# Kernel tuning notes

Measured on AMD Instinct MI355X. Metric: run time of the kernel, lower is better.

## Reference

```python
import jax, jax.numpy as jnp
import numpy as np

GRID_SIZE = 5
SPLINE_ORDER = 3
COUPLING = 0.05
LN_EPS = 1e-5
BATCH = 1024
IN_DIM = 2048
HIDDEN = [4096, 4096, 2048]


def _knots():
    k = SPLINE_ORDER
    return np.concatenate([np.full(k, -1.0), np.linspace(-1.0, 1.0, GRID_SIZE + 1), np.full(k, 1.0)])


def bspline_basis(t):
    # Replicates the module's partial in-place Cox-de Boor recursion exactly:
    # after the loops, cols[0..4] are degree-3, col 5 degree-2, col 6 degree-1, col 7 degree-0.
    knots = _knots()
    k = SPLINE_ORDER
    n = len(knots) - k - 1  # 8
    cols = [jnp.where((t >= knots[i]) & (t < knots[i + 1]), 1.0, 0.0).astype(t.dtype)
            for i in range(min(n, len(knots) - 1))]
    for degree in range(1, min(k + 1, n)):
        for i in range(n - degree):
            denom1 = knots[i + degree] - knots[i]
            denom2 = knots[i + degree + 1] - knots[i + 1]
            term1 = ((t - knots[i]) / denom1) * cols[i] if denom1 > 1e-10 else 0.0
            term2 = (((knots[i + degree + 1] - t) / denom2) * cols[i + 1]
                     if (denom2 > 1e-10 and i + 1 < n) else 0.0)
            cols[i] = term1 + term2
    return jnp.stack(cols, axis=-1)  # [..., n]


def kan_activation(x, control_points, reg_weights):
    # x: [B, D]; control_points: [D, grid+order+1]; reg_weights: [D]
    t = jnp.tanh(x)
    basis = bspline_basis(t)  # [B, D, n]
    m = min(basis.shape[-1], control_points.shape[1])  # min(8, 9) = 8
    spline = jnp.einsum('bdn,dn->bd', basis[..., :m], control_points[:, :m])
    return jnp.clip(spline * reg_weights[None, :], -10.0, 10.0)


def _generators():
    sx = np.array([[0., 1.], [1., 0.]], np.float32)
    sy = np.array([[0., -1.], [1., 0.]], np.float32)
    sz = np.array([[1., 0.], [0., -1.]], np.float32)
    return np.stack([sx, sy, sz, np.eye(2, dtype=np.float32)])  # [4,2,2]

GENS = jnp.asarray(_generators())
GEN_DIAG = jnp.asarray(np.stack([np.diagonal(g) for g in _generators()]))  # [4,2]


def noncommutative_transform(x):
    # pairs of the flattened tensor, generator index cycles mod 4
    shape = x.shape
    flat = x.reshape(-1)
    P = flat.shape[0] // 2
    vec = flat[:2 * P].reshape(P, 2)
    ng = GENS.shape[0]
    if P % ng == 0:
        v = vec.reshape(P // ng, ng, 2)                      # [Q, 4, 2]
        gv = jnp.einsum('gij,qgj->qgi', GENS, v)
        vg = v * GEN_DIAG[None, :, :]
        comm = jnp.clip(gv - vg, -1.0, 1.0)
        out = (v + COUPLING * comm).reshape(-1)
    else:
        G = GENS[jnp.arange(P) % ng]
        gv = jnp.einsum('pij,pj->pi', G, vec)
        vg = vec * jnp.diagonal(G, axis1=-2, axis2=-1)
        comm = jnp.clip(gv - vg, -1.0, 1.0)
        out = (vec + COUPLING * comm).reshape(-1)
    if flat.shape[0] % 2 == 1:
        out = jnp.concatenate([out, flat[-1:]])
    return out.reshape(shape)


def setup_inputs() -> dict:
    key = jax.random.key(0)
    ks = jax.random.split(key, 16)
    inp = {'x': jax.random.normal(ks[0], (BATCH, IN_DIM), jnp.float32)}
    prev = IN_DIM
    ncp = GRID_SIZE + SPLINE_ORDER + 1  # 9
    for li, h in enumerate(HIDDEN, start=1):
        kw, kb, kc = jax.random.split(ks[li], 3)
        inp[f'W{li}'] = jax.random.normal(kw, (h, prev), jnp.float32) / np.sqrt(prev)
        inp[f'b{li}'] = jnp.zeros((h,), jnp.float32)
        inp[f'cp{li}'] = jax.random.normal(kc, (h, ncp), jnp.float32) * 0.1
        inp[f'rw{li}'] = jnp.full((h,), 0.5, jnp.float32)
        prev = h
    inp['W_out'] = jax.random.normal(ks[10], (IN_DIM, prev), jnp.float32) / np.sqrt(prev)
    inp['b_out'] = jnp.zeros((IN_DIM,), jnp.float32)
    return inp


def reference(x, W1, b1, cp1, rw1, W2, b2, cp2, rw2, W3, b3, cp3, rw3, W_out, b_out):
    # F.layer_norm over feature dim, no affine
    mu = jnp.mean(x, axis=-1, keepdims=True)
    var = jnp.var(x, axis=-1, keepdims=True)
    cur = (x - mu) / jnp.sqrt(var + LN_EPS)
    for W, b, cp, rw in ((W1, b1, cp1, rw1), (W2, b2, cp2, rw2), (W3, b3, cp3, rw3)):
        lin = cur @ W.T + b
        kan = kan_activation(lin, cp, rw)
        cur = noncommutative_transform(kan)  # dropout = identity in eval
    return cur @ W_out.T + b_out
```

## Files before the change

### kernel.cpp

```cpp
#include <hip/hip_runtime.h>

typedef __attribute__((ext_vector_type(8))) short bf16x8;
typedef __attribute__((ext_vector_type(4))) float f32x4;

__device__ __forceinline__ float b2f(unsigned short u) {
    union { unsigned int i; float f; } x; x.i = ((unsigned int)u) << 16; return x.f;
}
__device__ __forceinline__ unsigned short f2b(float f) {
    union { float f; unsigned int i; } x; x.f = f;
    unsigned int r = x.i + 0x7fffu + ((x.i >> 16) & 1u);
    return (unsigned short)(r >> 16);
}

__device__ __forceinline__ void gl16(unsigned short* l, const unsigned short* g) {
    __builtin_amdgcn_global_load_lds((__attribute__((address_space(1))) void*)g,
                                     (__attribute__((address_space(3))) void*)l, 16, 0, 0);
}

__device__ __forceinline__ float kan_spline(float t, const float* cpf, float rwf) {
    float c3 = (t >= -1.0f && t < -0.6f) ? 1.0f : 0.0f;
    float c4 = (t >= -0.6f && t < -0.2f) ? 1.0f : 0.0f;
    float c5 = (t >= -0.2f && t <  0.2f) ? 1.0f : 0.0f;
    float c6 = (t >=  0.2f && t <  0.6f) ? 1.0f : 0.0f;
    float c7 = (t >=  0.6f && t <  1.0f) ? 1.0f : 0.0f;
    float d2 = (-0.6f - t) * 2.5f * c3;
    float d3 = (t + 1.0f) * 2.5f * c3 + (-0.2f - t) * 2.5f * c4;
    float d4 = (t + 0.6f) * 2.5f * c4 + ( 0.2f - t) * 2.5f * c5;
    float d5 = (t + 0.2f) * 2.5f * c5 + ( 0.6f - t) * 2.5f * c6;
    float d6 = (t - 0.2f) * 2.5f * c6 + ( 1.0f - t) * 2.5f * c7;
    float e1 = (-0.6f - t) * 2.5f  * d2;
    float e2 = (t + 1.0f) * 2.5f  * d2 + (-0.2f - t) * 1.25f * d3;
    float e3 = (t + 1.0f) * 1.25f * d3 + ( 0.2f - t) * 1.25f * d4;
    float e4 = (t + 0.6f) * 1.25f * d4 + ( 0.6f - t) * 1.25f * d5;
    float e5 = (t + 0.2f) * 1.25f * d5 + ( 1.0f - t) * 1.25f * d6;
    const float r12 = 1.0f / 1.2f;
    float f0 = (-0.6f - t) * 2.5f  * e1;
    float f1 = (t + 1.0f) * 2.5f  * e1 + (-0.2f - t) * 1.25f * e2;
    float f2 = (t + 1.0f) * 1.25f * e2 + ( 0.2f - t) * r12   * e3;
    float f3 = (t + 1.0f) * r12   * e3 + ( 0.6f - t) * r12   * e4;
    float f4 = (t + 0.6f) * r12   * e4 + ( 1.0f - t) * r12   * e5;
    float sp = f0*cpf[0] + f1*cpf[1] + f2*cpf[2] + f3*cpf[3] + f4*cpf[4]
             + e5*cpf[5] + d6*cpf[6] + c7*cpf[7];
    float v = sp * rwf;
    return fminf(fmaxf(v, -10.0f), 10.0f);
}

__global__ void ln_stats_kernel(const float* __restrict__ x,
                                float* __restrict__ mu, float* __restrict__ rstd) {
    const int row = blockIdx.x;
    const float* p = x + (size_t)row * 2048 + threadIdx.x * 8;
    double s = 0.0, q = 0.0;
#pragma unroll
    for (int i = 0; i < 8; ++i) { float v = p[i]; s += v; q += (double)v * v; }
    for (int o = 32; o > 0; o >>= 1) { s += __shfl_down(s, o, 64); q += __shfl_down(q, o, 64); }
    __shared__ double shs[4], shq[4];
    const int lane = threadIdx.x & 63, w = threadIdx.x >> 6;
    if (lane == 0) { shs[w] = s; shq[w] = q; }
    __syncthreads();
    if (threadIdx.x == 0) {
        double S = shs[0] + shs[1] + shs[2] + shs[3];
        double Q = shq[0] + shq[1] + shq[2] + shq[3];
        double m = S / 2048.0;
        double var = Q / 2048.0 - m * m;
        mu[row] = (float)m;
        rstd[row] = (float)(1.0 / sqrt(var + 1e-5));
    }
}

__global__ void rowsum_kernel(const float* __restrict__ W,
                              float* __restrict__ S, int K) {
    const int lane = threadIdx.x & 63, w = threadIdx.x >> 6;
    const int row = blockIdx.x * 4 + w;
    const float* p = W + (size_t)row * K;
    double s = 0.0;
    for (int c = lane * 8; c < K; c += 512) {
#pragma unroll
        for (int i = 0; i < 8; ++i) s += p[c + i];
    }
    for (int o = 32; o > 0; o >>= 1) s += __shfl_down(s, o, 64);
    if (lane == 0) S[row] = (float)s;
}

__global__ void split2_kernel(const float* __restrict__ src,
                              unsigned short* __restrict__ dst, int C) {
    const int r = blockIdx.x;
    const int c = threadIdx.x * 8;
    const float* p = src + (size_t)r * C + c;
    float4 u0 = ((const float4*)p)[0];
    float4 u1 = ((const float4*)p)[1];
    float v[8] = {u0.x, u0.y, u0.z, u0.w, u1.x, u1.y, u1.z, u1.w};
    unsigned short hi[8], lo[8];
#pragma unroll
    for (int i = 0; i < 8; ++i) {
        hi[i] = f2b(v[i]);
        lo[i] = f2b(v[i] - b2f(hi[i]));
    }
    unsigned short* d = dst + (size_t)r * 2 * C + c;
    *(uint4*)d = *(const uint4*)hi;
    *(uint4*)(d + C) = *(const uint4*)lo;
}

__global__ void cvt_kernel(const float* __restrict__ src,
                           unsigned short* __restrict__ dst) {
    const size_t i = ((size_t)blockIdx.x * 256 + threadIdx.x) * 8;
    float4 u0 = ((const float4*)(src + i))[0];
    float4 u1 = ((const float4*)(src + i))[1];
    float v[8] = {u0.x, u0.y, u0.z, u0.w, u1.x, u1.y, u1.z, u1.w};
    unsigned short t[8];
#pragma unroll
    for (int q = 0; q < 8; ++q) t[q] = f2b(v[q]);
    *(uint4*)(dst + i) = *(const uint4*)t;
}

template <int EPI>
__global__ __launch_bounds__(256, 2)
void gemm_kan2(const unsigned short* __restrict__ Ab,
               const unsigned short* __restrict__ Bb,
               const float* __restrict__ bias, const float* __restrict__ cp,
               const float* __restrict__ rw, const float* __restrict__ mu,
               const float* __restrict__ rstd, const float* __restrict__ S1,
               void* __restrict__ outp,
               int Nld, int n0, int Ktot, int lda, int ldb)
{
    constexpr int BM = 64, BN = 128, BK = 64;
    constexpr int ASZ = BM * BK;
    constexpr int BUF = ASZ + BN * BK;
    __shared__ unsigned short lds[3 * BUF];

    const int tid  = threadIdx.x;
    const int lane = tid & 63;
    const int wid  = tid >> 6;

    const int gx = gridDim.x;
    int flat = blockIdx.y * gx + blockIdx.x;
    const int nwg = gx * gridDim.y;
    if ((nwg & 7) == 0) flat = (flat & 7) * (nwg >> 3) + (flat >> 3);
    const int bm = (flat % gx) * BM;
    const int bn = (flat / gx) * BN;

    const int wmo = (wid >> 1) * 32;
    const int wno = (wid & 1) * 64;
    const int fr = lane & 15;
    const int kq = lane >> 4;
    const int sxr = fr & 7;

    const int uA0 = (wid << 7) + lane;
    const int uA1 = uA0 + 64;
    const int uB0 = (wid << 8) + lane;
    const int uB1 = uB0 + 64, uB2 = uB0 + 128, uB3 = uB0 + 192;
#define SRCOL(u) (((((u) & 7) ^ (((u) >> 3) & 7))) << 3)
    const size_t aoff0 = (size_t)(bm + (uA0 >> 3)) * lda + SRCOL(uA0);
    const size_t aoff1 = (size_t)(bm + (uA1 >> 3)) * lda + SRCOL(uA1);
    const size_t boff0 = (size_t)(bn + (uB0 >> 3)) * ldb + SRCOL(uB0);
    const size_t boff1 = (size_t)(bn + (uB1 >> 3)) * ldb + SRCOL(uB1);
    const size_t boff2 = (size_t)(bn + (uB2 >> 3)) * ldb + SRCOL(uB2);
    const size_t boff3 = (size_t)(bn + (uB3 >> 3)) * ldb + SRCOL(uB3);
#undef SRCOL

    f32x4 acc[2][4] = {};

#define STAGE(BSEL, AK, BKK) do {                                     \
    unsigned short* lA_ = &lds[(BSEL) * BUF];                         \
    unsigned short* lB_ = lA_ + ASZ;                                  \
    gl16(lA_ + uA0 * 8, Ab + aoff0 + (AK));                           \
    gl16(lA_ + uA1 * 8, Ab + aoff1 + (AK));                           \
    gl16(lB_ + uB0 * 8, Bb + boff0 + (BKK));                          \
    gl16(lB_ + uB1 * 8, Bb + boff1 + (BKK));                          \
    gl16(lB_ + uB2 * 8, Bb + boff2 + (BKK));                          \
    gl16(lB_ + uB3 * 8, Bb + boff3 + (BKK));                          \
} while (0)

    const int nt = Ktot / BK;
    STAGE(0, 0, 0);
    STAGE(1, BK, BK);

    for (int t = 0; t < nt; ++t) {
        if (t + 1 < nt) asm volatile("s_waitcnt vmcnt(6)" ::: "memory");
        else            asm volatile("s_waitcnt vmcnt(0)" ::: "memory");
        __builtin_amdgcn_s_barrier();
        __builtin_amdgcn_sched_barrier(0);
        if (t + 2 < nt) {
            const int kn = (t + 2) * BK;
            int ak = kn, bk = kn;
            if (EPI == 0) {
                ak = (kn < 4096) ? kn : kn - 4096;
                bk = (kn < 2048) ? kn : kn - 2048;
            }
            STAGE((t + 2) % 3, ak, bk);
        }
        const unsigned short* cl = &lds[(t % 3) * BUF];
#pragma unroll
        for (int s = 0; s < 2; ++s) {
            const int sl = ((((s << 2) + kq) ^ sxr)) << 3;
            bf16x8 aF[2], bF[4];
#pragma unroll
            for (int i = 0; i < 2; ++i)
                aF[i] = *(const bf16x8*)&cl[(wmo + i * 16 + fr) * BK + sl];
#pragma unroll
            for (int j = 0; j < 4; ++j)
                bF[j] = *(const bf16x8*)&cl[ASZ + (wno + j * 16 + fr) * BK + sl];
#pragma unroll
            for (int i = 0; i < 2; ++i)
#pragma unroll
                for (int j = 0; j < 4; ++j)
                    acc[i][j] = __builtin_amdgcn_mfma_f32_16x16x32_bf16(aF[i], bF[j], acc[i][j], 0, 0, 0);
        }
    }
#undef STAGE

    const int rowg = (lane >> 4) * 4;
#pragma unroll
    for (int j = 0; j < 4; ++j) {
        const int n = n0 + bn + wno + j * 16 + fr;
        const float bs = bias[n];
        float cpf[8], rwf = 0.0f, s1 = 0.0f;
        if (EPI < 2) {
#pragma unroll
            for (int q = 0; q < 8; ++q) cpf[q] = cp[(size_t)n * 9 + q];
            rwf = rw[n];
        }
        if (EPI == 0) s1 = S1[n];
        const int s = n & 7;
#pragma unroll
        for (int i = 0; i < 2; ++i) {
            const int m0 = bm + wmo + i * 16 + rowg;
#pragma unroll
            for (int r = 0; r < 4; ++r) {
                const int m = m0 + r;
                float v = acc[i][j][r];
                if (EPI == 0) v = (v - mu[m] * s1) * rstd[m] + bs;
                else          v += bs;
                if (EPI < 2) {
                    v = kan_spline(tanhf(v), cpf, rwf);
                    float p = __shfl_xor(v, 1, 64);
                    p = fminf(fmaxf(p, -1.0f), 1.0f);
                    if (s < 4) v += ((s == 2) ? -0.05f : 0.05f) * p;
                }
                if (EPI == 2) ((float*)outp)[(size_t)m * Nld + n] = v;
                else ((unsigned short*)outp)[(size_t)m * Nld + n] = f2b(v);
            }
        }
    }
}

template <int EPI, int BSRC>
__global__ __launch_bounds__(256, 2)
void gemm_kan(const void* __restrict__ Av, const void* __restrict__ Bv,
              const float* __restrict__ bias, const float* __restrict__ cp,
              const float* __restrict__ rw, const float* __restrict__ mu,
              const float* __restrict__ rstd, const float* __restrict__ S1,
              void* __restrict__ outp,
              int Nld, int n0, int Ktot, int lda, int ldb)
{
    constexpr int BM = 64, BN = 64, BK = 64, LDP = 72;
    constexpr bool SPL = (BSRC == 2);
    constexpr int OFF_B  = BM * LDP;
    constexpr int OFF_LO = (BM + BN) * LDP;
    __shared__ unsigned short lds[(SPL ? 2 : 1) * (BM + BN) * LDP];

    const int tid  = threadIdx.x;
    const int lane = tid & 63;
    const int wid  = tid >> 6;
    const int bm = blockIdx.x * BM;
    const int bn = blockIdx.y * BN;
    const int wmo = (wid >> 1) * 32;
    const int wno = (wid & 1) * 32;
    const int fr = lane & 15;
    const int kq = lane >> 4;
    const int sar = tid >> 3, sac = (tid & 7) << 3;
    const int sfr = tid >> 2, sfc = (tid & 3) << 4;

    f32x4 acc[2][2] = {};

    uint4 pA0 = {}, pA1 = {}, pB0 = {}, pB1 = {};
    const unsigned short* Ab = (const unsigned short*)Av;
    const unsigned short* Bb = (const unsigned short*)Bv;
    const size_t a0 = (size_t)(bm + sar) * lda + sac;
    const size_t a1 = (size_t)(bm + 32 + sar) * lda + sac;
    const size_t b0 = (size_t)(bn + sar) * ldb + sac;
    const size_t b1 = (size_t)(bn + 32 + sar) * ldb + sac;
    if constexpr (BSRC == 0) {
        pA0 = *(const uint4*)(Ab + a0);
        pA1 = *(const uint4*)(Ab + a1);
        pB0 = *(const uint4*)(Bb + b0);
        pB1 = *(const uint4*)(Bb + b1);
    }

    for (int k0 = 0; k0 < Ktot; k0 += BK) {
        if constexpr (BSRC == 0) {
            *(uint4*)&lds[sar * LDP + sac] = pA0;
            *(uint4*)&lds[(32 + sar) * LDP + sac] = pA1;
            *(uint4*)&lds[OFF_B + sar * LDP + sac] = pB0;
            *(uint4*)&lds[OFF_B + (32 + sar) * LDP + sac] = pB1;
        } else {
            {
                const float* g = (const float*)Bv + (size_t)(bn + sfr) * ldb + k0 + sfc;
                float4 u0 = ((const float4*)g)[0];
                float4 u1 = ((const float4*)g)[1];
                float4 u2 = ((const float4*)g)[2];
                float4 u3 = ((const float4*)g)[3];
                float v[16] = {u0.x,u0.y,u0.z,u0.w, u1.x,u1.y,u1.z,u1.w,
                               u2.x,u2.y,u2.z,u2.w, u3.x,u3.y,u3.z,u3.w};
                unsigned short hi[16], lo[16];
#pragma unroll
                for (int i = 0; i < 16; ++i) {
                    hi[i] = f2b(v[i]);
                    if (SPL) lo[i] = f2b(v[i] - b2f(hi[i]));
                }
                unsigned short* d = &lds[OFF_B + sfr * LDP + sfc];
                ((uint4*)d)[0] = *(const uint4*)&hi[0];
                ((uint4*)d)[1] = *(const uint4*)&hi[8];
                if constexpr (SPL) {
                    unsigned short* dl = d + OFF_LO;
                    ((uint4*)dl)[0] = *(const uint4*)&lo[0];
                    ((uint4*)dl)[1] = *(const uint4*)&lo[8];
                }
            }
            if constexpr (SPL) {
                const float* g = (const float*)Av + (size_t)(bm + sfr) * lda + k0 + sfc;
                float4 u0 = ((const float4*)g)[0];
                float4 u1 = ((const float4*)g)[1];
                float4 u2 = ((const float4*)g)[2];
                float4 u3 = ((const float4*)g)[3];
                float v[16] = {u0.x,u0.y,u0.z,u0.w, u1.x,u1.y,u1.z,u1.w,
                               u2.x,u2.y,u2.z,u2.w, u3.x,u3.y,u3.z,u3.w};
                unsigned short hi[16], lo[16];
#pragma unroll
                for (int i = 0; i < 16; ++i) {
                    hi[i] = f2b(v[i]);
                    lo[i] = f2b(v[i] - b2f(hi[i]));
                }
                unsigned short* d = &lds[sfr * LDP + sfc];
                ((uint4*)d)[0] = *(const uint4*)&hi[0];
                ((uint4*)d)[1] = *(const uint4*)&hi[8];
                unsigned short* dl = d + OFF_LO;
                ((uint4*)dl)[0] = *(const uint4*)&lo[0];
                ((uint4*)dl)[1] = *(const uint4*)&lo[8];
            } else {
                *(uint4*)&lds[sar * LDP + sac] = *(const uint4*)(Ab + a0 + k0);
                *(uint4*)&lds[(32 + sar) * LDP + sac] = *(const uint4*)(Ab + a1 + k0);
            }
        }
        __syncthreads();
        if constexpr (BSRC == 0) {
            if (k0 + BK < Ktot) {
                const int kn = k0 + BK;
                const int ak = (EPI == 0) ? (kn < 4096 ? kn : kn - 4096) : kn;
                const int bk = (EPI == 0) ? (kn < 2048 ? kn : kn - 2048) : kn;
                pA0 = *(const uint4*)(Ab + a0 + ak);
                pA1 = *(const uint4*)(Ab + a1 + ak);
                pB0 = *(const uint4*)(Bb + b0 + bk);
                pB1 = *(const uint4*)(Bb + b1 + bk);
            }
        }
#pragma unroll
        for (int s = 0; s < 2; ++s) {
            const int cc = (s * 4 + kq) << 3;
            bf16x8 aF[2], bF[2];
#pragma unroll
            for (int i = 0; i < 2; ++i)
                aF[i] = *(const bf16x8*)&lds[(wmo + i * 16 + fr) * LDP + cc];
#pragma unroll
            for (int j = 0; j < 2; ++j)
                bF[j] = *(const bf16x8*)&lds[OFF_B + (wno + j * 16 + fr) * LDP + cc];
#pragma unroll
            for (int i = 0; i < 2; ++i)
#pragma unroll
                for (int j = 0; j < 2; ++j)
                    acc[i][j] = __builtin_amdgcn_mfma_f32_16x16x32_bf16(aF[i], bF[j], acc[i][j], 0, 0, 0);
            if constexpr (SPL) {
                bf16x8 aL[2], bL[2];
#pragma unroll
                for (int i = 0; i < 2; ++i)
                    aL[i] = *(const bf16x8*)&lds[OFF_LO + (wmo + i * 16 + fr) * LDP + cc];
#pragma unroll
                for (int i = 0; i < 2; ++i)
#pragma unroll
                    for (int j = 0; j < 2; ++j)
                        acc[i][j] = __builtin_amdgcn_mfma_f32_16x16x32_bf16(aL[i], bF[j], acc[i][j], 0, 0, 0);
#pragma unroll
                for (int j = 0; j < 2; ++j)
                    bL[j] = *(const bf16x8*)&lds[OFF_LO + OFF_B + (wno + j * 16 + fr) * LDP + cc];
#pragma unroll
                for (int i = 0; i < 2; ++i)
#pragma unroll
                    for (int j = 0; j < 2; ++j)
                        acc[i][j] = __builtin_amdgcn_mfma_f32_16x16x32_bf16(aF[i], bL[j], acc[i][j], 0, 0, 0);
            }
        }
        __syncthreads();
    }

    const int rowg = (lane >> 4) * 4;
#pragma unroll
    for (int j = 0; j < 2; ++j) {
        const int n = n0 + bn + wno + j * 16 + fr;
        const float bs = bias[n];
        float cpf[8], rwf = 0.0f, s1 = 0.0f;
        if (EPI < 2) {
#pragma unroll
            for (int q = 0; q < 8; ++q) cpf[q] = cp[(size_t)n * 9 + q];
            rwf = rw[n];
        }
        if (EPI == 0) s1 = S1[n];
        const int s = n & 7;
#pragma unroll
        for (int i = 0; i < 2; ++i) {
            const int m0 = bm + wmo + i * 16 + rowg;
#pragma unroll
            for (int r = 0; r < 4; ++r) {
                const int m = m0 + r;
                float v = acc[i][j][r];
                if (EPI == 0) v = (v - mu[m] * s1) * rstd[m] + bs;
                else          v += bs;
                if (EPI < 2) {
                    v = kan_spline(tanhf(v), cpf, rwf);
                    float p = __shfl_xor(v, 1, 64);
                    p = fminf(fmaxf(p, -1.0f), 1.0f);
                    if (s < 4) v += ((s == 2) ? -0.05f : 0.05f) * p;
                }
                if (EPI == 2) ((float*)outp)[(size_t)m * Nld + n] = v;
                else ((unsigned short*)outp)[(size_t)m * Nld + n] = f2b(v);
            }
        }
    }
}

extern "C" void kernel_launch(void* const* d_in, const int* in_sizes, int n_in,
                              void* d_out, int out_size, void* d_ws, size_t ws_size,
                              hipStream_t stream) {
    const float* x    = (const float*)d_in[0];
    const float* W1   = (const float*)d_in[1];
    const float* b1   = (const float*)d_in[2];
    const float* cp1  = (const float*)d_in[3];
    const float* rw1  = (const float*)d_in[4];
    const float* W2   = (const float*)d_in[5];
    const float* b2   = (const float*)d_in[6];
    const float* cp2  = (const float*)d_in[7];
    const float* rw2  = (const float*)d_in[8];
    const float* W3   = (const float*)d_in[9];
    const float* b3   = (const float*)d_in[10];
    const float* cp3  = (const float*)d_in[11];
    const float* rw3  = (const float*)d_in[12];
    const float* Wout = (const float*)d_in[13];
    const float* bout = (const float*)d_in[14];

    char* ws = (char*)d_ws;
    float* mu   = (float*)(ws);
    float* rstd = (float*)(ws + 4096);
    float* S1   = (float*)(ws + 8192);
    unsigned short* A2 = (unsigned short*)(ws + 32768);
    unsigned short* A3 = (unsigned short*)(ws + 32768 + 8388608);
    unsigned short* A4 = A2;
    unsigned short* Asplit = A3;
    unsigned short* Wb = (unsigned short*)(ws + 32768 + 2 * 8388608);
    const size_t NEED_FULL = 32768 + 2 * 8388608 + 33554432;
    const size_t NEED_HALF = 32768 + 2 * 8388608 + 16777216;

    ln_stats_kernel<<<1024, 256, 0, stream>>>(x, mu, rstd);
    rowsum_kernel<<<1024, 256, 0, stream>>>(W1, S1, 2048);

    if (ws_size >= NEED_FULL) {
        split2_kernel<<<1024, 256, 0, stream>>>(x, Asplit, 2048);
        split2_kernel<<<4096, 256, 0, stream>>>(W1, Wb, 2048);
        gemm_kan2<0><<<dim3(16, 32), 256, 0, stream>>>(
            Asplit, Wb, b1, cp1, rw1, mu, rstd, S1, A2, 4096, 0, 6144, 4096, 4096);
        cvt_kernel<<<8192, 256, 0, stream>>>(W2, Wb);
        gemm_kan2<1><<<dim3(16, 32), 256, 0, stream>>>(
            A2, Wb, b2, cp2, rw2, nullptr, nullptr, nullptr, A3, 4096, 0, 4096, 4096, 4096);
        cvt_kernel<<<4096, 256, 0, stream>>>(W3, Wb);
        gemm_kan2<1><<<dim3(16, 16), 256, 0, stream>>>(
            A3, Wb, b3, cp3, rw3, nullptr, nullptr, nullptr, A4, 2048, 0, 4096, 4096, 4096);
        cvt_kernel<<<2048, 256, 0, stream>>>(Wout, Wb);
        gemm_kan2<2><<<dim3(16, 16), 256, 0, stream>>>(
            A4, Wb, bout, nullptr, nullptr, nullptr, nullptr, nullptr, d_out, 2048, 0, 2048, 2048, 2048);
    } else if (ws_size >= NEED_HALF) {
        split2_kernel<<<1024, 256, 0, stream>>>(x, Asplit, 2048);
        for (int h = 0; h < 2; ++h) {
            split2_kernel<<<2048, 256, 0, stream>>>(W1 + (size_t)h * 2048 * 2048, Wb, 2048);
            gemm_kan2<0><<<dim3(16, 16), 256, 0, stream>>>(
                Asplit, Wb, b1, cp1, rw1, mu, rstd, S1, A2, 4096, h * 2048, 6144, 4096, 4096);
        }
        for (int h = 0; h < 2; ++h) {
            cvt_kernel<<<4096, 256, 0, stream>>>(W2 + (size_t)h * 2048 * 4096, Wb);
            gemm_kan2<1><<<dim3(16, 16), 256, 0, stream>>>(
                A2, Wb, b2, cp2, rw2, nullptr, nullptr, nullptr, A3, 4096, h * 2048, 4096, 4096, 4096);
        }
        cvt_kernel<<<4096, 256, 0, stream>>>(W3, Wb);
        gemm_kan2<1><<<dim3(16, 16), 256, 0, stream>>>(
            A3, Wb, b3, cp3, rw3, nullptr, nullptr, nullptr, A4, 2048, 0, 4096, 4096, 4096);
        cvt_kernel<<<2048, 256, 0, stream>>>(Wout, Wb);
        gemm_kan2<2><<<dim3(16, 16), 256, 0, stream>>>(
            A4, Wb, bout, nullptr, nullptr, nullptr, nullptr, nullptr, d_out, 2048, 0, 2048, 2048, 2048);
    } else {
        gemm_kan<0, 2><<<dim3(16, 64), 256, 0, stream>>>(
            x, W1, b1, cp1, rw1, mu, rstd, S1, A2, 4096, 0, 2048, 2048, 2048);
        gemm_kan<1, 1><<<dim3(16, 64), 256, 0, stream>>>(
            A2, W2, b2, cp2, rw2, nullptr, nullptr, nullptr, A3, 4096, 0, 4096, 4096, 4096);
        gemm_kan<1, 1><<<dim3(16, 32), 256, 0, stream>>>(
            A3, W3, b3, cp3, rw3, nullptr, nullptr, nullptr, A4, 2048, 0, 4096, 4096, 4096);
        gemm_kan<2, 1><<<dim3(16, 32), 256, 0, stream>>>(
            A4, Wout, bout, nullptr, nullptr, nullptr, nullptr, nullptr, d_out, 2048, 0, 2048, 2048, 2048);
    }
}
```

Baseline: 395.8 us.

## Enlarge GEMM tile to 128x128 with double-buffered LDS pipeline

The bf16 GEMM+KAN kernel's M tile grows from 64 to 128, so each wave computes a 64x64 sub-tile with 16 MFMA accumulators and the grid halves in x. The LDS pipeline drops from three stages to two to fit the larger tile, and each iteration now waits for all outstanding loads (vmcnt(0)) before computing. The aim is more data reuse per LDS load and fewer workgroups re-reading B. The cost is more registers per thread, fewer workgroups, and less overlap between memory loads and compute.

```diff
diff --git a/kernel.cpp b/kernel.cpp
--- a/kernel.cpp
+++ b/kernel.cpp
@@ -114,7 +114,7 @@
 
 template <int EPI>
 __global__ __launch_bounds__(256, 2)
-void gemm_kan2(const unsigned short* __restrict__ Ab,
+void gemm_kan3(const unsigned short* __restrict__ Ab,
                const unsigned short* __restrict__ Bb,
                const float* __restrict__ bias, const float* __restrict__ cp,
                const float* __restrict__ rw, const float* __restrict__ mu,
@@ -122,10 +122,10 @@
                void* __restrict__ outp,
                int Nld, int n0, int Ktot, int lda, int ldb)
 {
-    constexpr int BM = 64, BN = 128, BK = 64;
+    constexpr int BM = 128, BN = 128, BK = 64;
     constexpr int ASZ = BM * BK;
     constexpr int BUF = ASZ + BN * BK;
-    __shared__ unsigned short lds[3 * BUF];
+    __shared__ unsigned short lds[2 * BUF];
 
     const int tid  = threadIdx.x;
     const int lane = tid & 63;
@@ -138,69 +138,69 @@
     const int bm = (flat % gx) * BM;
     const int bn = (flat / gx) * BN;
 
-    const int wmo = (wid >> 1) * 32;
+    const int wmo = (wid >> 1) * 64;
     const int wno = (wid & 1) * 64;
     const int fr = lane & 15;
     const int kq = lane >> 4;
     const int sxr = fr & 7;
 
-    const int uA0 = (wid << 7) + lane;
-    const int uA1 = uA0 + 64;
-    const int uB0 = (wid << 8) + lane;
-    const int uB1 = uB0 + 64, uB2 = uB0 + 128, uB3 = uB0 + 192;
+    const int u0 = (wid << 8) + lane;
+    const int u1 = u0 + 64, u2 = u0 + 128, u3 = u0 + 192;
 #define SRCOL(u) (((((u) & 7) ^ (((u) >> 3) & 7))) << 3)
-    const size_t aoff0 = (size_t)(bm + (uA0 >> 3)) * lda + SRCOL(uA0);
-    const size_t aoff1 = (size_t)(bm + (uA1 >> 3)) * lda + SRCOL(uA1);
-    const size_t boff0 = (size_t)(bn + (uB0 >> 3)) * ldb + SRCOL(uB0);
-    const size_t boff1 = (size_t)(bn + (uB1 >> 3)) * ldb + SRCOL(uB1);
-    const size_t boff2 = (size_t)(bn + (uB2 >> 3)) * ldb + SRCOL(uB2);
-    const size_t boff3 = (size_t)(bn + (uB3 >> 3)) * ldb + SRCOL(uB3);
+    const size_t aoff0 = (size_t)(bm + (u0 >> 3)) * lda + SRCOL(u0);
+    const size_t aoff1 = (size_t)(bm + (u1 >> 3)) * lda + SRCOL(u1);
+    const size_t aoff2 = (size_t)(bm + (u2 >> 3)) * lda + SRCOL(u2);
+    const size_t aoff3 = (size_t)(bm + (u3 >> 3)) * lda + SRCOL(u3);
+    const size_t boff0 = (size_t)(bn + (u0 >> 3)) * ldb + SRCOL(u0);
+    const size_t boff1 = (size_t)(bn + (u1 >> 3)) * ldb + SRCOL(u1);
+    const size_t boff2 = (size_t)(bn + (u2 >> 3)) * ldb + SRCOL(u2);
+    const size_t boff3 = (size_t)(bn + (u3 >> 3)) * ldb + SRCOL(u3);
 #undef SRCOL
 
-    f32x4 acc[2][4] = {};
+    f32x4 acc[4][4] = {};
 
 #define STAGE(BSEL, AK, BKK) do {                                     \
     unsigned short* lA_ = &lds[(BSEL) * BUF];                         \
     unsigned short* lB_ = lA_ + ASZ;                                  \
-    gl16(lA_ + uA0 * 8, Ab + aoff0 + (AK));                           \
-    gl16(lA_ + uA1 * 8, Ab + aoff1 + (AK));                           \
-    gl16(lB_ + uB0 * 8, Bb + boff0 + (BKK));                          \
-    gl16(lB_ + uB1 * 8, Bb + boff1 + (BKK));                          \
-    gl16(lB_ + uB2 * 8, Bb + boff2 + (BKK));                          \
-    gl16(lB_ + uB3 * 8, Bb + boff3 + (BKK));                          \
+    gl16(lA_ + u0 * 8, Ab + aoff0 + (AK));                            \
+    gl16(lA_ + u1 * 8, Ab + aoff1 + (AK));                            \
+    gl16(lA_ + u2 * 8, Ab + aoff2 + (AK));                            \
+    gl16(lA_ + u3 * 8, Ab + aoff3 + (AK));                            \
+    gl16(lB_ + u0 * 8, Bb + boff0 + (BKK));                           \
+    gl16(lB_ + u1 * 8, Bb + boff1 + (BKK));                           \
+    gl16(lB_ + u2 * 8, Bb + boff2 + (BKK));                           \
+    gl16(lB_ + u3 * 8, Bb + boff3 + (BKK));                           \
 } while (0)
 
     const int nt = Ktot / BK;
     STAGE(0, 0, 0);
-    STAGE(1, BK, BK);
 
     for (int t = 0; t < nt; ++t) {
-        if (t + 1 < nt) asm volatile("s_waitcnt vmcnt(6)" ::: "memory");
-        else            asm volatile("s_waitcnt vmcnt(0)" ::: "memory");
+        asm volatile("s_waitcnt vmcnt(0)" ::: "memory");
         __builtin_amdgcn_s_barrier();
         __builtin_amdgcn_sched_barrier(0);
-        if (t + 2 < nt) {
-            const int kn = (t + 2) * BK;
+        if (t + 1 < nt) {
+            const int kn = (t + 1) * BK;
             int ak = kn, bk = kn;
             if (EPI == 0) {
                 ak = (kn < 4096) ? kn : kn - 4096;
                 bk = (kn < 2048) ? kn : kn - 2048;
             }
-            STAGE((t + 2) % 3, ak, bk);
-        }
-        const unsigned short* cl = &lds[(t % 3) * BUF];
+            STAGE((t + 1) & 1, ak, bk);
+        }
+        const unsigned short* cl = &lds[(t & 1) * BUF];
 #pragma unroll
         for (int s = 0; s < 2; ++s) {
             const int sl = ((((s << 2) + kq) ^ sxr)) << 3;
-            bf16x8 aF[2], bF[4];
-#pragma unroll
-            for (int i = 0; i < 2; ++i)
+            bf16x8 aF[4], bF[4];
+#pragma unroll
+            for (int i = 0; i < 4; ++i)
                 aF[i] = *(const bf16x8*)&cl[(wmo + i * 16 + fr) * BK + sl];
 #pragma unroll
             for (int j = 0; j < 4; ++j)
                 bF[j] = *(const bf16x8*)&cl[ASZ + (wno + j * 16 + fr) * BK + sl];
 #pragma unroll
-            for (int i = 0; i < 2; ++i)
+            for (int i = 0; i < 4; ++i)
 #pragma unroll
                 for (int j = 0; j < 4; ++j)
                     acc[i][j] = __builtin_amdgcn_mfma_f32_16x16x32_bf16(aF[i], bF[j], acc[i][j], 0, 0, 0);
@@ -222,7 +222,7 @@
         if (EPI == 0) s1 = S1[n];
         const int s = n & 7;
 #pragma unroll
-        for (int i = 0; i < 2; ++i) {
+        for (int i = 0; i < 4; ++i) {
             const int m0 = bm + wmo + i * 16 + rowg;
 #pragma unroll
             for (int r = 0; r < 4; ++r) {
@@ -463,34 +463,34 @@
     if (ws_size >= NEED_FULL) {
         split2_kernel<<<1024, 256, 0, stream>>>(x, Asplit, 2048);
         split2_kernel<<<4096, 256, 0, stream>>>(W1, Wb, 2048);
-        gemm_kan2<0><<<dim3(16, 32), 256, 0, stream>>>(
+        gemm_kan3<0><<<dim3(8, 32), 256, 0, stream>>>(
             Asplit, Wb, b1, cp1, rw1, mu, rstd, S1, A2, 4096, 0, 6144, 4096, 4096);
         cvt_kernel<<<8192, 256, 0, stream>>>(W2, Wb);
-        gemm_kan2<1><<<dim3(16, 32), 256, 0, stream>>>(
+        gemm_kan3<1><<<dim3(8, 32), 256, 0, stream>>>(
             A2, Wb, b2, cp2, rw2, nullptr, nullptr, nullptr, A3, 4096, 0, 4096, 4096, 4096);
         cvt_kernel<<<4096, 256, 0, stream>>>(W3, Wb);
-        gemm_kan2<1><<<dim3(16, 16), 256, 0, stream>>>(
+        gemm_kan3<1><<<dim3(8, 16), 256, 0, stream>>>(
             A3, Wb, b3, cp3, rw3, nullptr, nullptr, nullptr, A4, 2048, 0, 4096, 4096, 4096);
         cvt_kernel<<<2048, 256, 0, stream>>>(Wout, Wb);
-        gemm_kan2<2><<<dim3(16, 16), 256, 0, stream>>>(
+        gemm_kan3<2><<<dim3(8, 16), 256, 0, stream>>>(
             A4, Wb, bout, nullptr, nullptr, nullptr, nullptr, nullptr, d_out, 2048, 0, 2048, 2048, 2048);
     } else if (ws_size >= NEED_HALF) {
         split2_kernel<<<1024, 256, 0, stream>>>(x, Asplit, 2048);
         for (int h = 0; h < 2; ++h) {
             split2_kernel<<<2048, 256, 0, stream>>>(W1 + (size_t)h * 2048 * 2048, Wb, 2048);
-            gemm_kan2<0><<<dim3(16, 16), 256, 0, stream>>>(
+            gemm_kan3<0><<<dim3(8, 16), 256, 0, stream>>>(
                 Asplit, Wb, b1, cp1, rw1, mu, rstd, S1, A2, 4096, h * 2048, 6144, 4096, 4096);
         }
         for (int h = 0; h < 2; ++h) {
             cvt_kernel<<<4096, 256, 0, stream>>>(W2 + (size_t)h * 2048 * 4096, Wb);
-            gemm_kan2<1><<<dim3(16, 16), 256, 0, stream>>>(
+            gemm_kan3<1><<<dim3(8, 16), 256, 0, stream>>>(
                 A2, Wb, b2, cp2, rw2, nullptr, nullptr, nullptr, A3, 4096, h * 2048, 4096, 4096, 4096);
         }
         cvt_kernel<<<4096, 256, 0, stream>>>(W3, Wb);
-        gemm_kan2<1><<<dim3(16, 16), 256, 0, stream>>>(
+        gemm_kan3<1><<<dim3(8, 16), 256, 0, stream>>>(
             A3, Wb, b3, cp3, rw3, nullptr, nullptr, nullptr, A4, 2048, 0, 4096, 4096, 4096);
         cvt_kernel<<<2048, 256, 0, stream>>>(Wout, Wb);
-        gemm_kan2<2><<<dim3(16, 16), 256, 0, stream>>>(
+        gemm_kan3<2><<<dim3(8, 16), 256, 0, stream>>>(
             A4, Wb, bout, nullptr, nullptr, nullptr, nullptr, nullptr, d_out, 2048, 0, 2048, 2048, 2048);
     } else {
         gemm_kan<0, 2><<<dim3(16, 64), 256, 0, stream>>>(
```

New measurement: 460.7 us. +16.4%, slower.

## Split-K the last two GEMMs with separate reduce+KAN epilogue kernel

Applied to the files above, without the earlier changes.

Layers 3 and output GEMMs now split K into two halves, doubling workgroup count, writing fp32 partials that a new reduce_epi kernel sums and applies bias, KAN spline and pair coupling. The goal is to fill more CUs on the small-N GEMMs. The main loop also rotates LDS buffer offsets instead of computing modulos, and raises wave priority around the MFMA block. This adds extra partial-sum traffic and two extra launches.

```diff
diff --git a/kernel.cpp b/kernel.cpp
--- a/kernel.cpp
+++ b/kernel.cpp
@@ -112,6 +112,47 @@
     *(uint4*)(dst + i) = *(const uint4*)t;
 }
 
+template <int RK>
+__global__ void reduce_epi(const float* __restrict__ P, const float* __restrict__ bias,
+                           const float* __restrict__ cp, const float* __restrict__ rw,
+                           void* __restrict__ outp, int N) {
+    const int m = blockIdx.x;
+    const int c0 = threadIdx.x * 8;
+    const float* p0 = P + (size_t)m * N + c0;
+    const float* p1 = P + (size_t)(1024 + m) * N + c0;
+    float4 a0 = ((const float4*)p0)[0], a1 = ((const float4*)p0)[1];
+    float4 b0 = ((const float4*)p1)[0], b1 = ((const float4*)p1)[1];
+    float v[8] = {a0.x + b0.x, a0.y + b0.y, a0.z + b0.z, a0.w + b0.w,
+                  a1.x + b1.x, a1.y + b1.y, a1.z + b1.z, a1.w + b1.w};
+#pragma unroll
+    for (int i = 0; i < 8; ++i) v[i] += bias[c0 + i];
+    if constexpr (RK == 1) {
+        float w[8];
+#pragma unroll
+        for (int i = 0; i < 8; ++i) {
+            const int n = c0 + i;
+            float cpf[8];
+#pragma unroll
+            for (int q = 0; q < 8; ++q) cpf[q] = cp[(size_t)n * 9 + q];
+            w[i] = kan_spline(tanhf(v[i]), cpf, rw[n]);
+        }
+        unsigned short o[8];
+#pragma unroll
+        for (int i = 0; i < 8; ++i) {
+            float val = w[i];
+            const int s = i;
+            float p = fminf(fmaxf(w[i ^ 1], -1.0f), 1.0f);
+            if (s < 4) val += ((s == 2) ? -0.05f : 0.05f) * p;
+            o[i] = f2b(val);
+        }
+        *(uint4*)((unsigned short*)outp + (size_t)m * N + c0) = *(const uint4*)o;
+    } else {
+        float* o = (float*)outp + (size_t)m * N + c0;
+        ((float4*)o)[0] = make_float4(v[0], v[1], v[2], v[3]);
+        ((float4*)o)[1] = make_float4(v[4], v[5], v[6], v[7]);
+    }
+}
+
 template <int EPI>
 __global__ __launch_bounds__(256, 2)
 void gemm_kan2(const unsigned short* __restrict__ Ab,
@@ -120,7 +161,7 @@
                const float* __restrict__ rw, const float* __restrict__ mu,
                const float* __restrict__ rstd, const float* __restrict__ S1,
                void* __restrict__ outp,
-               int Nld, int n0, int Ktot, int lda, int ldb)
+               int Nld, int n0, int Ktot, int lda, int ldb, int nbn)
 {
     constexpr int BM = 64, BN = 128, BK = 64;
     constexpr int ASZ = BM * BK;
@@ -136,7 +177,10 @@
     const int nwg = gx * gridDim.y;
     if ((nwg & 7) == 0) flat = (flat & 7) * (nwg >> 3) + (flat >> 3);
     const int bm = (flat % gx) * BM;
-    const int bn = (flat / gx) * BN;
+    const int rest = flat / gx;
+    const int bn = (rest % nbn) * BN;
+    const int kh = rest / nbn;
+    const int koff = kh * Ktot;
 
     const int wmo = (wid >> 1) * 32;
     const int wno = (wid & 1) * 64;
@@ -149,18 +193,18 @@
     const int uB0 = (wid << 8) + lane;
     const int uB1 = uB0 + 64, uB2 = uB0 + 128, uB3 = uB0 + 192;
 #define SRCOL(u) (((((u) & 7) ^ (((u) >> 3) & 7))) << 3)
-    const size_t aoff0 = (size_t)(bm + (uA0 >> 3)) * lda + SRCOL(uA0);
-    const size_t aoff1 = (size_t)(bm + (uA1 >> 3)) * lda + SRCOL(uA1);
-    const size_t boff0 = (size_t)(bn + (uB0 >> 3)) * ldb + SRCOL(uB0);
-    const size_t boff1 = (size_t)(bn + (uB1 >> 3)) * ldb + SRCOL(uB1);
-    const size_t boff2 = (size_t)(bn + (uB2 >> 3)) * ldb + SRCOL(uB2);
-    const size_t boff3 = (size_t)(bn + (uB3 >> 3)) * ldb + SRCOL(uB3);
+    const size_t aoff0 = (size_t)(bm + (uA0 >> 3)) * lda + SRCOL(uA0) + koff;
+    const size_t aoff1 = (size_t)(bm + (uA1 >> 3)) * lda + SRCOL(uA1) + koff;
+    const size_t boff0 = (size_t)(bn + (uB0 >> 3)) * ldb + SRCOL(uB0) + koff;
+    const size_t boff1 = (size_t)(bn + (uB1 >> 3)) * ldb + SRCOL(uB1) + koff;
+    const size_t boff2 = (size_t)(bn + (uB2 >> 3)) * ldb + SRCOL(uB2) + koff;
+    const size_t boff3 = (size_t)(bn + (uB3 >> 3)) * ldb + SRCOL(uB3) + koff;
 #undef SRCOL
 
     f32x4 acc[2][4] = {};
 
-#define STAGE(BSEL, AK, BKK) do {                                     \
-    unsigned short* lA_ = &lds[(BSEL) * BUF];                         \
+#define STAGE(OFF, AK, BKK) do {                                      \
+    unsigned short* lA_ = &lds[(OFF)];                                \
     unsigned short* lB_ = lA_ + ASZ;                                  \
     gl16(lA_ + uA0 * 8, Ab + aoff0 + (AK));                           \
     gl16(lA_ + uA1 * 8, Ab + aoff1 + (AK));                           \
@@ -171,8 +215,9 @@
 } while (0)
 
     const int nt = Ktot / BK;
-    STAGE(0, 0, 0);
-    STAGE(1, BK, BK);
+    unsigned int o0 = 0, o1 = BUF, o2 = 2u * BUF;
+    STAGE(o0, 0, 0);
+    STAGE(o1, BK, BK);
 
     for (int t = 0; t < nt; ++t) {
         if (t + 1 < nt) asm volatile("s_waitcnt vmcnt(6)" ::: "memory");
@@ -182,13 +227,14 @@
         if (t + 2 < nt) {
             const int kn = (t + 2) * BK;
             int ak = kn, bk = kn;
-            if (EPI == 0) {
+            if constexpr (EPI == 0) {
                 ak = (kn < 4096) ? kn : kn - 4096;
                 bk = (kn < 2048) ? kn : kn - 2048;
             }
-            STAGE((t + 2) % 3, ak, bk);
-        }
-        const unsigned short* cl = &lds[(t % 3) * BUF];
+            STAGE(o2, ak, bk);
+        }
+        const unsigned short* cl = &lds[o0];
+        __builtin_amdgcn_s_setprio(1);
 #pragma unroll
         for (int s = 0; s < 2; ++s) {
             const int sl = ((((s << 2) + kq) ^ sxr)) << 3;
@@ -205,6 +251,8 @@
                 for (int j = 0; j < 4; ++j)
                     acc[i][j] = __builtin_amdgcn_mfma_f32_16x16x32_bf16(aF[i], bF[j], acc[i][j], 0, 0, 0);
         }
+        __builtin_amdgcn_s_setprio(0);
+        const unsigned int tmp = o0; o0 = o1; o1 = o2; o2 = tmp;
     }
 #undef STAGE
 
@@ -212,14 +260,14 @@
 #pragma unroll
     for (int j = 0; j < 4; ++j) {
         const int n = n0 + bn + wno + j * 16 + fr;
-        const float bs = bias[n];
-        float cpf[8], rwf = 0.0f, s1 = 0.0f;
-        if (EPI < 2) {
+        float bs = 0.0f, cpf[8], rwf = 0.0f, s1 = 0.0f;
+        if constexpr (EPI < 3) bs = bias[n];
+        if constexpr (EPI < 2) {
 #pragma unroll
             for (int q = 0; q < 8; ++q) cpf[q] = cp[(size_t)n * 9 + q];
             rwf = rw[n];
         }
-        if (EPI == 0) s1 = S1[n];
+        if constexpr (EPI == 0) s1 = S1[n];
         const int s = n & 7;
 #pragma unroll
         for (int i = 0; i < 2; ++i) {
@@ -228,15 +276,16 @@
             for (int r = 0; r < 4; ++r) {
                 const int m = m0 + r;
                 float v = acc[i][j][r];
-                if (EPI == 0) v = (v - mu[m] * s1) * rstd[m] + bs;
-                else          v += bs;
-                if (EPI < 2) {
+                if constexpr (EPI == 0) v = (v - mu[m] * s1) * rstd[m] + bs;
+                else if constexpr (EPI < 3) v += bs;
+                if constexpr (EPI < 2) {
                     v = kan_spline(tanhf(v), cpf, rwf);
                     float p = __shfl_xor(v, 1, 64);
                     p = fminf(fmaxf(p, -1.0f), 1.0f);
                     if (s < 4) v += ((s == 2) ? -0.05f : 0.05f) * p;
                 }
-                if (EPI == 2) ((float*)outp)[(size_t)m * Nld + n] = v;
+                if constexpr (EPI == 2)      ((float*)outp)[(size_t)m * Nld + n] = v;
+                else if constexpr (EPI == 3) ((float*)outp)[(size_t)(kh * 1024 + m) * Nld + n] = v;
                 else ((unsigned short*)outp)[(size_t)m * Nld + n] = f2b(v);
             }
         }
@@ -454,6 +503,7 @@
     unsigned short* A4 = A2;
     unsigned short* Asplit = A3;
     unsigned short* Wb = (unsigned short*)(ws + 32768 + 2 * 8388608);
+    float* Pk = (float*)(ws + 32768 + 2 * 8388608 + 16777216);
     const size_t NEED_FULL = 32768 + 2 * 8388608 + 33554432;
     const size_t NEED_HALF = 32768 + 2 * 8388608 + 16777216;
 
@@ -464,34 +514,36 @@
         split2_kernel<<<1024, 256, 0, stream>>>(x, Asplit, 2048);
         split2_kernel<<<4096, 256, 0, stream>>>(W1, Wb, 2048);
         gemm_kan2<0><<<dim3(16, 32), 256, 0, stream>>>(
-            Asplit, Wb, b1, cp1, rw1, mu, rstd, S1, A2, 4096, 0, 6144, 4096, 4096);
+            Asplit, Wb, b1, cp1, rw1, mu, rstd, S1, A2, 4096, 0, 6144, 4096, 4096, 32);
         cvt_kernel<<<8192, 256, 0, stream>>>(W2, Wb);
         gemm_kan2<1><<<dim3(16, 32), 256, 0, stream>>>(
-            A2, Wb, b2, cp2, rw2, nullptr, nullptr, nullptr, A3, 4096, 0, 4096, 4096, 4096);
+            A2, Wb, b2, cp2, rw2, nullptr, nullptr, nullptr, A3, 4096, 0, 4096, 4096, 4096, 32);
         cvt_kernel<<<4096, 256, 0, stream>>>(W3, Wb);
-        gemm_kan2<1><<<dim3(16, 16), 256, 0, stream>>>(
-            A3, Wb, b3, cp3, rw3, nullptr, nullptr, nullptr, A4, 2048, 0, 4096, 4096, 4096);
+        gemm_kan2<3><<<dim3(16, 32), 256, 0, stream>>>(
+            A3, Wb, nullptr, nullptr, nullptr, nullptr, nullptr, nullptr, Pk, 2048, 0, 2048, 4096, 4096, 16);
+        reduce_epi<1><<<1024, 256, 0, stream>>>(Pk, b3, cp3, rw3, A4, 2048);
         cvt_kernel<<<2048, 256, 0, stream>>>(Wout, Wb);
-        gemm_kan2<2><<<dim3(16, 16), 256, 0, stream>>>(
-            A4, Wb, bout, nullptr, nullptr, nullptr, nullptr, nullptr, d_out, 2048, 0, 2048, 2048, 2048);
+        gemm_kan2<3><<<dim3(16, 32), 256, 0, stream>>>(
+            A4, Wb, nullptr, nullptr, nullptr, nullptr, nullptr, nullptr, Pk, 2048, 0, 1024, 2048, 2048, 16);
+        reduce_epi<2><<<1024, 256, 0, stream>>>(Pk, bout, nullptr, nullptr, d_out, 2048);
     } else if (ws_size >= NEED_HALF) {
         split2_kernel<<<1024, 256, 0, stream>>>(x, Asplit, 2048);
         for (int h = 0; h < 2; ++h) {
             split2_kernel<<<2048, 256, 0, stream>>>(W1 + (size_t)h * 2048 * 2048, Wb, 2048);
             gemm_kan2<0><<<dim3(16, 16), 256, 0, stream>>>(
-                Asplit, Wb, b1, cp1, rw1, mu, rstd, S1, A2, 4096, h * 2048, 6144, 4096, 4096);
+                Asplit, Wb, b1, cp1, rw1, mu, rstd, S1, A2, 4096, h * 2048, 6144, 4096, 4096, 16);
         }
         for (int h = 0; h < 2; ++h) {
             cvt_kernel<<<4096, 256, 0, stream>>>(W2 + (size_t)h * 2048 * 4096, Wb);
             gemm_kan2<1><<<dim3(16, 16), 256, 0, stream>>>(
-                A2, Wb, b2, cp2, rw2, nullptr, nullptr, nullptr, A3, 4096, h * 2048, 4096, 4096, 4096);
+                A2, Wb, b2, cp2, rw2, nullptr, nullptr, nullptr, A3, 4096, h * 2048, 4096, 4096, 4096, 16);
         }
         cvt_kernel<<<4096, 256, 0, stream>>>(W3, Wb);
         gemm_kan2<1><<<dim3(16, 16), 256, 0, stream>>>(
-            A3, Wb, b3, cp3, rw3, nullptr, nullptr, nullptr, A4, 2048, 0, 4096, 4096, 4096);
+            A3, Wb, b3, cp3, rw3, nullptr, nullptr, nullptr, A4, 2048, 0, 4096, 4096, 4096, 16);
         cvt_kernel<<<2048, 256, 0, stream>>>(Wout, Wb);
         gemm_kan2<2><<<dim3(16, 16), 256, 0, stream>>>(
-            A4, Wb, bout, nullptr, nullptr, nullptr, nullptr, nullptr, d_out, 2048, 0, 2048, 2048, 2048);
+            A4, Wb, bout, nullptr, nullptr, nullptr, nullptr, nullptr, d_out, 2048, 0, 2048, 2048, 2048, 16);
     } else {
         gemm_kan<0, 2><<<dim3(16, 64), 256, 0, stream>>>(
             x, W1, b1, cp1, rw1, mu, rstd, S1, A2, 4096, 0, 2048, 2048, 2048);
```

Result: no change. 402.0 us (+1.6%).
